# Performance work log

Measured on AMD Instinct MI355X. Metric: run time of the kernel, lower is better.

Reference implementation:

```python
import jax, jax.numpy as jnp
import numpy as np

G, P, PO, TAU = 4, 32, 128, 2.0  # n_groups, spatial_points, out_points=P*out_multiplier, level-softmax temperature
STRIDES = (4.0, 8.0, 16.0, 32.0)
EPS = 1e-5

def _ln2(x):
    # LayerNorm over last two dims, no affine (F.layer_norm(x, x.shape[-2:]))
    mu = jnp.mean(x, axis=(-2, -1), keepdims=True)
    var = jnp.var(x, axis=(-2, -1), keepdims=True)
    return (x - mu) * jax.lax.rsqrt(var + EPS)

def _ln1(x, g, b):
    mu = jnp.mean(x, axis=-1, keepdims=True)
    var = jnp.var(x, axis=-1, keepdims=True)
    return (x - mu) * jax.lax.rsqrt(var + EPS) * g + b

def _bilinear(feat, xp, yp):
    # feat: (B,G,H,W,Ce); xp,yp: (B,N,G,P) pixel coords; grid_sample bilinear,
    # zero padding, align_corners=False semantics.
    B, Gg, H, W, Ce = feat.shape
    x0 = jnp.floor(xp); y0 = jnp.floor(yp)
    wx1 = xp - x0; wy1 = yp - y0
    b_idx = jnp.arange(B)[:, None, None, None]
    g_idx = jnp.arange(Gg)[None, None, :, None]
    def gather(xi, yi):
        valid = (xi >= 0) & (xi < W) & (yi >= 0) & (yi < H)
        xc = jnp.clip(xi, 0, W - 1).astype(jnp.int32)
        yc = jnp.clip(yi, 0, H - 1).astype(jnp.int32)
        return feat[b_idx, g_idx, yc, xc] * valid[..., None]
    v00 = gather(x0, y0); v10 = gather(x0 + 1.0, y0)
    v01 = gather(x0, y0 + 1.0); v11 = gather(x0 + 1.0, y0 + 1.0)
    wx0 = 1.0 - wx1; wy0 = 1.0 - wy1
    return (v00 * (wx0 * wy0)[..., None] + v10 * (wx1 * wy0)[..., None]
            + v01 * (wx0 * wy1)[..., None] + v11 * (wx1 * wy1)[..., None])

def _forward(queries, xyzr, feats, W_off, b_off, W_param, b_param, W_out, b_out, gamma, beta):
    B, N, D = queries.shape
    Ce = feats[0].shape[1] // G  # 64 channels per group
    # learned offsets -> sample points (make_sample_points)
    offset = (queries @ W_off + b_off).reshape(B, N, G, P, 3)
    xy = xyzr[..., :2]
    z = xyzr[..., 2]
    r = xyzr[..., 3:4]
    roi_wh = (2.0 ** xyzr[..., 2:3]) * (2.0 ** jnp.concatenate([-0.5 * r, 0.5 * r], axis=-1))  # (B,N,2)
    sample_xy = xy[:, :, None, None, :] + offset[..., :2] * roi_wh[:, :, None, None, :]  # (B,N,G,P,2)
    sample_z = z[:, :, None, None] + offset[..., 2]  # (B,N,G,P) log2 scale
    # soft level assignment across the FPN pyramid
    lvl_log = jnp.log2(jnp.asarray(STRIDES, dtype=queries.dtype))
    lw = jax.nn.softmax(-((sample_z[..., None] - lvl_log) ** 2) / TAU, axis=-1)  # (B,N,G,P,L)
    # SAMPLE4D (image mode, T=1): multi-scale group-wise bilinear gather, level-weighted sum
    sampled = jnp.zeros((B, N, G, P, Ce), queries.dtype)
    for l, feat in enumerate(feats):
        H, W = feat.shape[-2:]
        featg = feat.reshape(B, G, Ce, H, W).transpose(0, 1, 3, 4, 2)  # (B,G,H,W,Ce)
        xp = sample_xy[..., 0] / STRIDES[l] - 0.5
        yp = sample_xy[..., 1] / STRIDES[l] - 0.5
        sampled = sampled + _bilinear(featg, xp, yp) * lw[..., l, None]
    # AdaptiveMixing: per-query generated channel-mix M and point-mix S
    params = (queries @ W_param + b_param).reshape(B, N, G, -1)
    M = params[..., :Ce * Ce].reshape(B, N, G, Ce, Ce)
    S = params[..., Ce * Ce:].reshape(B, N, G, PO, P)
    h = jnp.einsum('bngpc,bngcd->bngpd', sampled, M)  # channel mixing
    h = jax.nn.relu(_ln2(h))
    h = jnp.einsum('bngqp,bngpd->bngqd', S, h)        # point mixing -> (B,N,G,PO,Ce)
    h = jax.nn.relu(_ln2(h))
    h = h.reshape(B, N, G * PO * Ce)
    q = queries + h @ W_out + b_out  # out_proj + residual
    return _ln1(q, gamma, beta)      # norm_s

def setup_inputs() -> dict:
    key = jax.random.key(0)
    ks = jax.random.split(key, 12)
    B, N, D, C = 2, 300, 256, 256
    HW = [(200, 336), (100, 168), (50, 84), (25, 42)]
    inp = {}
    inp['queries'] = jax.random.normal(ks[0], (B, N, D), jnp.float32)
    u = jax.random.uniform(ks[1], (B, N, 4), jnp.float32)
    inp['xyzr'] = jnp.stack([u[..., 0] * 1344.0, u[..., 1] * 800.0,
                             2.0 + 3.0 * u[..., 2], u[..., 3] - 0.5], axis=-1)
    for i, (H, W) in enumerate(HW):
        inp[f'feat{i}'] = jax.random.normal(ks[2 + i], (B, C, H, W), jnp.float32)
    npar = G * (64 * 64 + PO * P)  # 32768
    inp['W_off'] = jax.random.normal(ks[6], (D, G * P * 3), jnp.float32) * 0.02
    inp['b_off'] = jax.random.normal(ks[7], (G * P * 3,), jnp.float32) * 0.1
    inp['W_param'] = jax.random.normal(ks[8], (D, npar), jnp.float32) * (1.0 / np.sqrt(D))
    inp['b_param'] = jnp.zeros((npar,), jnp.float32)
    inp['W_out'] = jax.random.normal(ks[9], (G * PO * 64, D), jnp.float32) * (1.0 / np.sqrt(G * PO * 64))
    inp['b_out'] = jnp.zeros((D,), jnp.float32)
    inp['gamma'] = jnp.ones((D,), jnp.float32)
    inp['beta'] = jnp.zeros((D,), jnp.float32)
    return inp

def reference(queries, xyzr, feat0, feat1, feat2, feat3, W_off, b_off, W_param, b_param, W_out, b_out, gamma, beta):
    return _forward(queries, xyzr, (feat0, feat1, feat2, feat3),
                    W_off, b_off, W_param, b_param, W_out, b_out, gamma, beta)
```

## Files before the change

### kernel.cpp

```cpp
#include <hip/hip_runtime.h>
#include <hip/hip_bf16.h>

typedef short bf16x8 __attribute__((ext_vector_type(8)));
typedef float f32x4 __attribute__((ext_vector_type(4)));
typedef unsigned short u16x4 __attribute__((ext_vector_type(4)));

#define NQ 600
#define D 256
#define NPAR 32768
#define EPS 1e-5f
#define KSPLIT 32

#define OFF_OFFS     ((size_t)0)
#define OFF_QB       ((size_t)1048576)
#define OFF_WOFFT    ((size_t)1441792)
#define OFF_H        ((size_t)2097152)
#define OFF_WPT      ((size_t)2097152)
#define OFF_PARAMS   ((size_t)41418752)
#define OFF_KPART    ((size_t)41418752)
#define OFF_WOT      ((size_t)80740352)
#define OFF_FEATT    ((size_t)97517568)

#define PIX_PER_BG 89250

__device__ __forceinline__ void gload_lds16(const void* g, void* l) {
    __builtin_amdgcn_global_load_lds((const __attribute__((address_space(1))) unsigned int*)g,
                                     (__attribute__((address_space(3))) unsigned int*)l,
                                     16, 0, 0);
}
__device__ __forceinline__ float bf2f(unsigned short us) {
    union { unsigned u; float f; } cv; cv.u = ((unsigned)us) << 16; return cv.f;
}
__device__ __forceinline__ unsigned short f2bf(float f) {
    __hip_bfloat16 h = __float2bfloat16(f);
    return *(unsigned short*)&h;
}

__global__ __launch_bounds__(256) void k_feat(
        const float* __restrict__ f0, const float* __restrict__ f1,
        const float* __restrict__ f2, const float* __restrict__ f3,
        __hip_bfloat16* __restrict__ featT) {
    int bid = blockIdx.x;
    int bg = bid / 349, wblk = bid % 349;
    int t = threadIdx.x, lane = t & 63, w = t >> 6;
    int wid = wblk * 4 + w;
    const float* in; int HW, lvloff, wstart;
    if (wid < 1050)      { in = f0; HW = 67200; lvloff = 0;     wstart = 0; }
    else if (wid < 1313) { in = f1; HW = 16800; lvloff = 67200; wstart = 1050; }
    else if (wid < 1379) { in = f2; HW = 4200;  lvloff = 84000; wstart = 1313; }
    else                 { in = f3; HW = 1050;  lvloff = 88200; wstart = 1379; }
    int b = bg >> 2, g = bg & 3;
    int pix = (wid - wstart) * 64 + lane;
    bool ok = pix < HW;
    int pixc = ok ? pix : HW - 1;
    const float* base = in + (size_t)(b * 256 + g * 64) * HW + pixc;
    float v[64];
    #pragma unroll
    for (int c = 0; c < 64; c++) v[c] = base[(size_t)c * HW];
    if (ok) {
        __hip_bfloat16* ob = featT + ((size_t)bg * PIX_PER_BG + lvloff + pixc) * 64;
        #pragma unroll
        for (int s8 = 0; s8 < 8; s8++) {
            unsigned short o[8];
            #pragma unroll
            for (int i = 0; i < 8; i++) o[i] = f2bf(v[s8 * 8 + i]);
            *(bf16x8*)(ob + s8 * 8) = *(bf16x8*)o;
        }
    }
}

__global__ __launch_bounds__(256) void k_wprep(
        const float* __restrict__ W_param, const float* __restrict__ W_out,
        const float* __restrict__ W_off, const float* __restrict__ q,
        __hip_bfloat16* __restrict__ Wpt, __hip_bfloat16* __restrict__ Wot,
        __hip_bfloat16* __restrict__ Wofft, __hip_bfloat16* __restrict__ qb) {
    __shared__ float tile[32][33];
    int idx = blockIdx.x;
    int t = threadIdx.x;
    if (idx >= 16480) {
        int i = (idx - 16480) * 2048 + t * 8;
        float4 v0 = *(const float4*)(q + i);
        float4 v1 = *(const float4*)(q + i + 4);
        unsigned short o[8];
        o[0] = f2bf(v0.x); o[1] = f2bf(v0.y); o[2] = f2bf(v0.z); o[3] = f2bf(v0.w);
        o[4] = f2bf(v1.x); o[5] = f2bf(v1.y); o[6] = f2bf(v1.z); o[7] = f2bf(v1.w);
        *(bf16x8*)(qb + i) = *(bf16x8*)o;
        return;
    }
    const float* in; __hip_bfloat16* out; int R, C, bx, by;
    if (idx < 8192)       { in = W_param; out = Wpt;   R = 256;   C = 32768; bx = idx & 1023; by = idx >> 10; }
    else if (idx < 16384) { idx -= 8192;  in = W_out;  out = Wot; R = 32768; C = 256; bx = idx & 7; by = idx >> 3; }
    else                  { idx -= 16384; in = W_off;  out = Wofft; R = 256; C = 384; bx = idx % 12; by = idx / 12; }
    int tx = t & 31, ty = t >> 5;
    int c = bx * 32 + tx;
    #pragma unroll
    for (int i = 0; i < 4; i++) {
        int rr = by * 32 + ty + i * 8;
        float v = 0.f;
        if (rr < R && c < C) v = in[(size_t)rr * C + c];
        tile[ty + i * 8][tx] = v;
    }
    __syncthreads();
    int r2 = by * 32 + tx;
    #pragma unroll
    for (int i = 0; i < 4; i++) {
        int c2 = bx * 32 + ty + i * 8;
        if (c2 < C && r2 < R) out[(size_t)c2 * R + r2] = __float2bfloat16(tile[tx][ty + i * 8]);
    }
}

__global__ __launch_bounds__(256) void k_gemm1_offs(const __hip_bfloat16* __restrict__ A,
                              const __hip_bfloat16* __restrict__ WofftB, const __hip_bfloat16* __restrict__ WptB,
                              const float* __restrict__ b_off, const float* __restrict__ b_param,
                              float* __restrict__ offs, __hip_bfloat16* __restrict__ params) {
    __shared__ __align__(16) char ldsB[32768];
    int id = blockIdx.x;
    bool isOff = id < 30;
    int m0, n0;
    const __hip_bfloat16* Bt;
    const float* bias;
    if (isOff) { m0 = (id % 5) * 128; n0 = (id / 5) * 64; Bt = WofftB; bias = b_off; }
    else { int i2 = id - 30; m0 = (i2 % 5) * 128; n0 = (i2 / 5) * 64; Bt = WptB; bias = b_param; }
    int t = threadIdx.x;
    int lane = t & 63, w = t >> 6;
    int la = lane & 15, lb = lane >> 4;

    const char* Bg = (const char*)Bt;
    #pragma unroll
    for (int r = 0; r < 8; r++) {
        int p = (r * 4 + w) * 64 + lane;
        int row = p >> 5, c16 = p & 31;
        int c16s = c16 ^ (row & 7);
        gload_lds16(Bg + (size_t)(n0 + row) * 512 + c16s * 16, ldsB + p * 16);
    }
    bf16x8 a[2][8];
    #pragma unroll
    for (int mi = 0; mi < 2; mi++) {
        int row = m0 + w * 32 + mi * 16 + la;
        row = row < NQ ? row : NQ - 1;
        #pragma unroll
        for (int ks = 0; ks < 8; ks++)
            a[mi][ks] = *(const bf16x8*)(A + (size_t)row * 256 + ks * 32 + lb * 8);
    }
    f32x4 acc[2][4];
    #pragma unroll
    for (int i = 0; i < 2; i++)
        #pragma unroll
        for (int j = 0; j < 4; j++) acc[i][j] = (f32x4)(0.f);
    __syncthreads();

    #pragma unroll
    for (int ks = 0; ks < 8; ks++) {
        bf16x8 b[4];
        #pragma unroll
        for (int ni = 0; ni < 4; ni++) {
            int row = ni * 16 + la;
            int c16s = (ks * 4 + lb) ^ (row & 7);
            b[ni] = *(const bf16x8*)(ldsB + row * 512 + c16s * 16);
        }
        #pragma unroll
        for (int mi = 0; mi < 2; mi++)
            #pragma unroll
            for (int ni = 0; ni < 4; ni++)
                acc[mi][ni] = __builtin_amdgcn_mfma_f32_16x16x32_bf16(a[mi][ks], b[ni], acc[mi][ni], 0, 0, 0);
    }
    #pragma unroll
    for (int mi = 0; mi < 2; mi++) {
        int rbase = m0 + w * 32 + mi * 16 + lb * 4;
        #pragma unroll
        for (int ni = 0; ni < 4; ni++) {
            int col = n0 + ni * 16 + la;
            float bv = bias[col];
            #pragma unroll
            for (int rg = 0; rg < 4; rg++) {
                int row = rbase + rg;
                if (row < NQ) {
                    if (isOff) offs[(size_t)row * 384 + col] = acc[mi][ni][rg] + bv;
                    else params[(size_t)row * NPAR + col] = __float2bfloat16(acc[mi][ni][rg] + bv);
                }
            }
        }
    }
}

#define MIX_SMP 0
#define MIX_MT  4096
#define MIX_SS  12288
#define MIX_H1T 20480
__device__ inline float2 blk_reduce2(float s, float ss, float* red, float norm) {
    __syncthreads();
    #pragma unroll
    for (int off = 32; off; off >>= 1) { s += __shfl_down(s, off); ss += __shfl_down(ss, off); }
    int wave = threadIdx.x >> 6, lane = threadIdx.x & 63;
    if (lane == 0) { red[wave * 2] = s; red[wave * 2 + 1] = ss; }
    __syncthreads();
    if (threadIdx.x == 0) {
        float a = 0.f, b = 0.f;
        #pragma unroll
        for (int i = 0; i < 4; i++) { a += red[2 * i]; b += red[2 * i + 1]; }
        red[8] = a * norm; red[9] = b * norm;
    }
    __syncthreads();
    return make_float2(red[8], red[9]);
}

__global__ __launch_bounds__(256) void k_sample_mix(const float* __restrict__ offs,
                      const float* __restrict__ xyzr,
                      const __hip_bfloat16* __restrict__ featT,
                      const __hip_bfloat16* __restrict__ params,
                      __hip_bfloat16* __restrict__ h) {
    __shared__ __align__(16) char lds[24576];
    __shared__ float smeta[32][8];
    __shared__ float red[16];
    int bid = blockIdx.x;
    int m = bid >> 2, g = bid & 3;
    int b = m / 300;
    int t = threadIdx.x;
    int lane = t & 63, w = t >> 6;
    int la = lane & 15, lb = lane >> 4;
    const __hip_bfloat16* pbase = params + (size_t)m * NPAR + g * 8192;

    #pragma unroll
    for (int r = 0; r < 2; r++) {
        int i = t + r * 256;
        int c = i >> 3, d0 = (i & 7) * 8;
        bf16x8 v = *(const bf16x8*)(pbase + i * 8);
        #pragma unroll
        for (int j = 0; j < 8; j++) {
            int d = d0 + j;
            int addr = MIX_MT + d * 128 + ((c >> 3) ^ (d & 7)) * 16 + (c & 7) * 2;
            *(unsigned short*)(lds + addr) = ((unsigned short*)&v)[j];
        }
    }
    #pragma unroll
    for (int r = 0; r < 2; r++) {
        int i = t + r * 256;
        int qr = i >> 2, c16 = i & 3;
        bf16x8 v = *(const bf16x8*)(pbase + 4096 + i * 8);
        *(bf16x8*)(lds + MIX_SS + qr * 64 + (c16 ^ (qr & 3)) * 16) = v;
    }
    if (t < 32) {
        int p = t;
        const float* op = offs + (size_t)m * 384 + (g * 32 + p) * 3;
        float o0 = op[0], o1 = op[1], o2 = op[2];
        float cx = xyzr[m * 4 + 0], cy = xyzr[m * 4 + 1], z = xyzr[m * 4 + 2], rr = xyzr[m * 4 + 3];
        smeta[p][0] = cx + o0 * exp2f(z - 0.5f * rr);
        smeta[p][1] = cy + o1 * exp2f(z + 0.5f * rr);
        float sz = z + o2;
        float e[4], mx = -1e30f;
        #pragma unroll
        for (int l = 0; l < 4; l++) { float d = sz - (float)(2 + l); e[l] = -0.5f * d * d; mx = fmaxf(mx, e[l]); }
        float ssum = 0.f;
        #pragma unroll
        for (int l = 0; l < 4; l++) { e[l] = __expf(e[l] - mx); ssum += e[l]; }
        float inv = 1.f / ssum;
        #pragma unroll
        for (int l = 0; l < 4; l++) smeta[p][2 + l] = e[l] * inv;
    }
    __syncthreads();

    int corner = lane >> 4;
    int dx = corner & 1, dy = corner >> 1;
    int ch = (lane & 15) * 4;
    const int Hs[4] = {200, 100, 50, 25};
    const int Ws[4] = {336, 168, 84, 42};
    const int Ls[4] = {0, 67200, 84000, 88200};
    const float invS[4] = {0.25f, 0.125f, 0.0625f, 0.03125f};
    const __hip_bfloat16* base_bg = featT + (size_t)(b * 4 + g) * PIX_PER_BG * 64;
    for (int pi = 0; pi < 8; pi++) {
        int p = w * 8 + pi;
        float sx = smeta[p][0], sy = smeta[p][1];
        float acc0 = 0.f, acc1 = 0.f, acc2 = 0.f, acc3 = 0.f;
        #pragma unroll
        for (int l = 0; l < 4; l++) {
            float wl = smeta[p][2 + l];
            if (wl < 1e-6f) continue;
            const int H = Hs[l], W = Ws[l];
            float xp = sx * invS[l] - 0.5f, yp = sy * invS[l] - 0.5f;
            float x0f = floorf(xp), y0f = floorf(yp);
            float wx1 = xp - x0f, wy1 = yp - y0f;
            int xi = (int)x0f + dx, yi = (int)y0f + dy;
            bool valid = (xi >= 0) && (xi < W) && (yi >= 0) && (yi < H);
            int xc = xi < 0 ? 0 : (xi >= W ? W - 1 : xi);
            int yc = yi < 0 ? 0 : (yi >= H ? H - 1 : yi);
            float cw = (dx ? wx1 : 1.f - wx1) * (dy ? wy1 : 1.f - wy1) * wl;
            if (!valid) cw = 0.f;
            const __hip_bfloat16* src = base_bg + ((size_t)Ls[l] + (size_t)yc * W + xc) * 64 + ch;
            u16x4 v = *(const u16x4*)src;
            acc0 += cw * bf2f(v[0]);
            acc1 += cw * bf2f(v[1]);
            acc2 += cw * bf2f(v[2]);
            acc3 += cw * bf2f(v[3]);
        }
        acc0 += __shfl_xor(acc0, 16); acc1 += __shfl_xor(acc1, 16);
        acc2 += __shfl_xor(acc2, 16); acc3 += __shfl_xor(acc3, 16);
        acc0 += __shfl_xor(acc0, 32); acc1 += __shfl_xor(acc1, 32);
        acc2 += __shfl_xor(acc2, 32); acc3 += __shfl_xor(acc3, 32);
        if (lane < 16) {
            unsigned short o[4];
            o[0] = f2bf(acc0); o[1] = f2bf(acc1); o[2] = f2bf(acc2); o[3] = f2bf(acc3);
            int slot = lane >> 1, half = lane & 1;
            *(u16x4*)(lds + MIX_SMP + p * 128 + ((slot ^ (p & 7)) * 16) + half * 8) = *(u16x4*)o;
        }
    }
    __syncthreads();

    f32x4 acc1v[2];
    acc1v[0] = (f32x4)(0.f); acc1v[1] = (f32x4)(0.f);
    int dcol = w * 16 + la;
    #pragma unroll
    for (int ks = 0; ks < 2; ks++) {
        bf16x8 bfr = *(const bf16x8*)(lds + MIX_MT + dcol * 128 + (((ks * 4 + lb)) ^ (dcol & 7)) * 16);
        #pragma unroll
        for (int mi = 0; mi < 2; mi++) {
            int prow = mi * 16 + la;
            bf16x8 afr = *(const bf16x8*)(lds + MIX_SMP + prow * 128 + ((ks * 4 + lb) ^ (prow & 7)) * 16);
            acc1v[mi] = __builtin_amdgcn_mfma_f32_16x16x32_bf16(afr, bfr, acc1v[mi], 0, 0, 0);
        }
    }
    float s = 0.f, ss = 0.f;
    #pragma unroll
    for (int mi = 0; mi < 2; mi++)
        #pragma unroll
        for (int j = 0; j < 4; j++) { float v = acc1v[mi][j]; s += v; ss += v * v; }
    float2 r1 = blk_reduce2(s, ss, red, 1.f / 2048.f);
    float mu = r1.x, inv = rsqrtf(r1.y - r1.x * r1.x + EPS);
    #pragma unroll
    for (int mi = 0; mi < 2; mi++) {
        u16x4 pk;
        #pragma unroll
        for (int rg = 0; rg < 4; rg++) {
            float v = (acc1v[mi][rg] - mu) * inv;
            pk[rg] = f2bf(v > 0.f ? v : 0.f);
        }
        int c16 = mi * 2 + (lb >> 1);
        int off8 = 8 * (lb & 1);
        *(u16x4*)(lds + MIX_H1T + dcol * 64 + ((c16 ^ (dcol & 3)) * 16) + off8) = pk;
    }
    __syncthreads();

    f32x4 acc2v[8];
    bf16x8 bfr2 = *(const bf16x8*)(lds + MIX_H1T + dcol * 64 + ((lb ^ (dcol & 3)) * 16));
    #pragma unroll
    for (int nj = 0; nj < 8; nj++) {
        int qrow = nj * 16 + la;
        bf16x8 afr = *(const bf16x8*)(lds + MIX_SS + qrow * 64 + ((lb ^ (qrow & 3)) * 16));
        acc2v[nj] = __builtin_amdgcn_mfma_f32_16x16x32_bf16(afr, bfr2, (f32x4)(0.f), 0, 0, 0);
    }
    s = 0.f; ss = 0.f;
    #pragma unroll
    for (int nj = 0; nj < 8; nj++)
        #pragma unroll
        for (int j = 0; j < 4; j++) { float v = acc2v[nj][j]; s += v; ss += v * v; }
    float2 r2 = blk_reduce2(s, ss, red, 1.f / 8192.f);
    float mu2 = r2.x, inv2 = rsqrtf(r2.y - r2.x * r2.x + EPS);
    __hip_bfloat16* hb = h + (size_t)m * NPAR + g * 8192;
    #pragma unroll
    for (int nj = 0; nj < 8; nj++) {
        #pragma unroll
        for (int rg = 0; rg < 4; rg++) {
            int qr = nj * 16 + lb * 4 + rg;
            float v = (acc2v[nj][rg] - mu2) * inv2;
            v = v > 0.f ? v : 0.f;
            hb[qr * 64 + dcol] = __float2bfloat16(v);
        }
    }
}

__global__ __launch_bounds__(256) void k_gemm_out(const __hip_bfloat16* __restrict__ A,
                           const __hip_bfloat16* __restrict__ Bt, float* __restrict__ kpart) {
    __shared__ __align__(16) char lds[49152];
    int bid = blockIdx.x;
    int work = (bid & 7) * 80 + (bid >> 3);
    int mblk = work % 10;
    int nz = work / 10;
    int n0 = (nz & 1) * 128;
    int z = nz >> 1;
    int m0 = mblk * 64;
    size_t k0 = (size_t)z * 1024;
    int t = threadIdx.x, lane = t & 63, w = t >> 6;
    int la = lane & 15, lb = lane >> 4;
    int wm = w >> 1, wn = w & 1;

    const char* Ag = (const char*)A;
    const char* Bg = (const char*)Bt;

    auto stage = [&](int buf, int st) {
        size_t kk = k0 + (size_t)st * 64;
        char* dstA = lds + buf * 24576;
        char* dstB = dstA + 8192;
        #pragma unroll
        for (int r = 0; r < 2; r++) {
            int p = (r * 4 + w) * 64 + lane;
            int row = p >> 3, c16 = p & 7;
            int c16s = c16 ^ (row & 7);
            int grow = m0 + row; grow = grow < NQ ? grow : NQ - 1;
            gload_lds16(Ag + ((size_t)grow * NPAR + kk) * 2 + c16s * 16, dstA + p * 16);
        }
        #pragma unroll
        for (int r = 0; r < 4; r++) {
            int p = (r * 4 + w) * 64 + lane;
            int row = p >> 3, c16 = p & 7;
            int c16s = c16 ^ (row & 7);
            gload_lds16(Bg + ((size_t)(n0 + row) * NPAR + kk) * 2 + c16s * 16, dstB + p * 16);
        }
    };

    f32x4 acc[2][4];
    #pragma unroll
    for (int i = 0; i < 2; i++)
        #pragma unroll
        for (int j = 0; j < 4; j++) acc[i][j] = (f32x4)(0.f);

    stage(0, 0);
    __syncthreads();
    for (int st = 0; st < 16; st++) {
        int buf = st & 1;
        if (st < 15) stage(buf ^ 1, st + 1);
        const char* tA = lds + buf * 24576;
        const char* tB = tA + 8192;
        #pragma unroll
        for (int ks = 0; ks < 2; ks++) {
            bf16x8 a[2], b[4];
            #pragma unroll
            for (int mi = 0; mi < 2; mi++) {
                int row = wm * 32 + mi * 16 + la;
                int c16s = (ks * 4 + lb) ^ (row & 7);
                a[mi] = *(const bf16x8*)(tA + row * 128 + c16s * 16);
            }
            #pragma unroll
            for (int ni = 0; ni < 4; ni++) {
                int row = wn * 64 + ni * 16 + la;
                int c16s = (ks * 4 + lb) ^ (row & 7);
                b[ni] = *(const bf16x8*)(tB + row * 128 + c16s * 16);
            }
            #pragma unroll
            for (int mi = 0; mi < 2; mi++)
                #pragma unroll
                for (int ni = 0; ni < 4; ni++)
                    acc[mi][ni] = __builtin_amdgcn_mfma_f32_16x16x32_bf16(a[mi], b[ni], acc[mi][ni], 0, 0, 0);
        }
        __syncthreads();
    }

    float* outp = kpart + (size_t)z * (NQ * D);
    #pragma unroll
    for (int mi = 0; mi < 2; mi++) {
        int rbase = m0 + wm * 32 + mi * 16 + lb * 4;
        #pragma unroll
        for (int ni = 0; ni < 4; ni++) {
            int col = n0 + wn * 64 + ni * 16 + la;
            #pragma unroll
            for (int rg = 0; rg < 4; rg++) {
                int row = rbase + rg;
                if (row < NQ) outp[(size_t)row * D + col] = acc[mi][ni][rg];
            }
        }
    }
}

__global__ void k_ln_out(const float* __restrict__ kpart, const float* __restrict__ queries,
                         const float* __restrict__ b_out, const float* __restrict__ gamma,
                         const float* __restrict__ beta, float* __restrict__ out) {
    int m = blockIdx.x, t = threadIdx.x;
    float x = queries[m * 256 + t] + b_out[t];
    for (int kc = 0; kc < KSPLIT; kc++) x += kpart[(size_t)kc * (NQ * D) + m * 256 + t];
    __shared__ float red[16];
    float s = x, ss = x * x;
    #pragma unroll
    for (int off = 32; off; off >>= 1) { s += __shfl_down(s, off); ss += __shfl_down(ss, off); }
    int wave = t >> 6, lane = t & 63;
    if (lane == 0) { red[wave * 2] = s; red[wave * 2 + 1] = ss; }
    __syncthreads();
    if (t == 0) {
        float a = 0.f, b = 0.f;
        #pragma unroll
        for (int i = 0; i < 4; i++) { a += red[2 * i]; b += red[2 * i + 1]; }
        red[8] = a * (1.f / 256.f); red[9] = b * (1.f / 256.f);
    }
    __syncthreads();
    float mu = red[8], var = red[9] - mu * mu;
    float inv = rsqrtf(var + EPS);
    out[m * 256 + t] = (x - mu) * inv * gamma[t] + beta[t];
}

extern "C" void kernel_launch(void* const* d_in, const int* in_sizes, int n_in,
                              void* d_out, int out_size, void* d_ws, size_t ws_size,
                              hipStream_t stream) {
    const float* queries = (const float*)d_in[0];
    const float* xyzr    = (const float*)d_in[1];
    const float* f0      = (const float*)d_in[2];
    const float* f1      = (const float*)d_in[3];
    const float* f2      = (const float*)d_in[4];
    const float* f3      = (const float*)d_in[5];
    const float* W_off   = (const float*)d_in[6];
    const float* b_off   = (const float*)d_in[7];
    const float* W_param = (const float*)d_in[8];
    const float* b_param = (const float*)d_in[9];
    const float* W_out   = (const float*)d_in[10];
    const float* b_out   = (const float*)d_in[11];
    const float* gamma   = (const float*)d_in[12];
    const float* beta    = (const float*)d_in[13];
    float* out = (float*)d_out;
    char* ws = (char*)d_ws;

    float* offs            = (float*)(ws + OFF_OFFS);
    __hip_bfloat16* qb     = (__hip_bfloat16*)(ws + OFF_QB);
    __hip_bfloat16* Wofft  = (__hip_bfloat16*)(ws + OFF_WOFFT);
    __hip_bfloat16* hbuf   = (__hip_bfloat16*)(ws + OFF_H);
    __hip_bfloat16* Wpt    = (__hip_bfloat16*)(ws + OFF_WPT);
    __hip_bfloat16* params = (__hip_bfloat16*)(ws + OFF_PARAMS);
    float* kpart           = (float*)(ws + OFF_KPART);
    __hip_bfloat16* Wot    = (__hip_bfloat16*)(ws + OFF_WOT);
    __hip_bfloat16* featT  = (__hip_bfloat16*)(ws + OFF_FEATT);

    k_feat<<<2792, 256, 0, stream>>>(f0, f1, f2, f3, featT);
    k_wprep<<<16555, 256, 0, stream>>>(W_param, W_out, W_off, queries, Wpt, Wot, Wofft, qb);
    k_gemm1_offs<<<2590, 256, 0, stream>>>(qb, Wofft, Wpt, b_off, b_param, offs, params);
    k_sample_mix<<<2400, 256, 0, stream>>>(offs, xyzr, featT, params, hbuf);
    k_gemm_out<<<640, 256, 0, stream>>>(hbuf, Wot, kpart);
    k_ln_out<<<600, 256, 0, stream>>>(kpart, queries, b_out, gamma, beta, out);
}
```

Before: 205.0 us.

## Fuse weight transpose into GEMM1 and merge feature and weight prep kernels

```diff
diff --git a/kernel.cpp b/kernel.cpp
--- a/kernel.cpp
+++ b/kernel.cpp
@@ -13,9 +13,7 @@
 
 #define OFF_OFFS     ((size_t)0)
 #define OFF_QB       ((size_t)1048576)
-#define OFF_WOFFT    ((size_t)1441792)
 #define OFF_H        ((size_t)2097152)
-#define OFF_WPT      ((size_t)2097152)
 #define OFF_PARAMS   ((size_t)41418752)
 #define OFF_KPART    ((size_t)41418752)
 #define OFF_WOT      ((size_t)80740352)
@@ -36,147 +34,148 @@
     return *(unsigned short*)&h;
 }
 
-__global__ __launch_bounds__(256) void k_feat(
+__global__ __launch_bounds__(256) void k_prep(
         const float* __restrict__ f0, const float* __restrict__ f1,
         const float* __restrict__ f2, const float* __restrict__ f3,
-        __hip_bfloat16* __restrict__ featT) {
+        const float* __restrict__ W_out, const float* __restrict__ q,
+        __hip_bfloat16* __restrict__ featT,
+        __hip_bfloat16* __restrict__ Wot, __hip_bfloat16* __restrict__ qb) {
+    __shared__ float tile[32][33];
     int bid = blockIdx.x;
-    int bg = bid / 349, wblk = bid % 349;
-    int t = threadIdx.x, lane = t & 63, w = t >> 6;
-    int wid = wblk * 4 + w;
-    const float* in; int HW, lvloff, wstart;
-    if (wid < 1050)      { in = f0; HW = 67200; lvloff = 0;     wstart = 0; }
-    else if (wid < 1313) { in = f1; HW = 16800; lvloff = 67200; wstart = 1050; }
-    else if (wid < 1379) { in = f2; HW = 4200;  lvloff = 84000; wstart = 1313; }
-    else                 { in = f3; HW = 1050;  lvloff = 88200; wstart = 1379; }
-    int b = bg >> 2, g = bg & 3;
-    int pix = (wid - wstart) * 64 + lane;
-    bool ok = pix < HW;
-    int pixc = ok ? pix : HW - 1;
-    const float* base = in + (size_t)(b * 256 + g * 64) * HW + pixc;
-    float v[64];
-    #pragma unroll
-    for (int c = 0; c < 64; c++) v[c] = base[(size_t)c * HW];
-    if (ok) {
-        __hip_bfloat16* ob = featT + ((size_t)bg * PIX_PER_BG + lvloff + pixc) * 64;
-        #pragma unroll
-        for (int s8 = 0; s8 < 8; s8++) {
-            unsigned short o[8];
-            #pragma unroll
-            for (int i = 0; i < 8; i++) o[i] = f2bf(v[s8 * 8 + i]);
-            *(bf16x8*)(ob + s8 * 8) = *(bf16x8*)o;
-        }
-    }
-}
-
-__global__ __launch_bounds__(256) void k_wprep(
-        const float* __restrict__ W_param, const float* __restrict__ W_out,
-        const float* __restrict__ W_off, const float* __restrict__ q,
-        __hip_bfloat16* __restrict__ Wpt, __hip_bfloat16* __restrict__ Wot,
-        __hip_bfloat16* __restrict__ Wofft, __hip_bfloat16* __restrict__ qb) {
-    __shared__ float tile[32][33];
-    int idx = blockIdx.x;
     int t = threadIdx.x;
-    if (idx >= 16480) {
-        int i = (idx - 16480) * 2048 + t * 8;
-        float4 v0 = *(const float4*)(q + i);
-        float4 v1 = *(const float4*)(q + i + 4);
-        unsigned short o[8];
-        o[0] = f2bf(v0.x); o[1] = f2bf(v0.y); o[2] = f2bf(v0.z); o[3] = f2bf(v0.w);
-        o[4] = f2bf(v1.x); o[5] = f2bf(v1.y); o[6] = f2bf(v1.z); o[7] = f2bf(v1.w);
-        *(bf16x8*)(qb + i) = *(bf16x8*)o;
+    if (bid < 2792) {
+        int bg = bid / 349, wblk = bid % 349;
+        int lane = t & 63, w = t >> 6;
+        int wid = wblk * 4 + w;
+        const float* in; int HW, lvloff, wstart;
+        if (wid < 1050)      { in = f0; HW = 67200; lvloff = 0;     wstart = 0; }
+        else if (wid < 1313) { in = f1; HW = 16800; lvloff = 67200; wstart = 1050; }
+        else if (wid < 1379) { in = f2; HW = 4200;  lvloff = 84000; wstart = 1313; }
+        else                 { in = f3; HW = 1050;  lvloff = 88200; wstart = 1379; }
+        int b = bg >> 2, g = bg & 3;
+        int pix = (wid - wstart) * 64 + lane;
+        bool ok = pix < HW;
+        int pixc = ok ? pix : HW - 1;
+        const float* base = in + (size_t)(b * 256 + g * 64) * HW + pixc;
+        float v[64];
+        #pragma unroll
+        for (int c = 0; c < 64; c++) v[c] = base[(size_t)c * HW];
+        if (ok) {
+            __hip_bfloat16* ob = featT + ((size_t)bg * PIX_PER_BG + lvloff + pixc) * 64;
+            #pragma unroll
+            for (int s8 = 0; s8 < 8; s8++) {
+                unsigned short o[8];
+                #pragma unroll
+                for (int i = 0; i < 8; i++) o[i] = f2bf(v[s8 * 8 + i]);
+                *(bf16x8*)(ob + s8 * 8) = *(bf16x8*)o;
+            }
+        }
         return;
     }
-    const float* in; __hip_bfloat16* out; int R, C, bx, by;
-    if (idx < 8192)       { in = W_param; out = Wpt;   R = 256;   C = 32768; bx = idx & 1023; by = idx >> 10; }
-    else if (idx < 16384) { idx -= 8192;  in = W_out;  out = Wot; R = 32768; C = 256; bx = idx & 7; by = idx >> 3; }
-    else                  { idx -= 16384; in = W_off;  out = Wofft; R = 256; C = 384; bx = idx % 12; by = idx / 12; }
-    int tx = t & 31, ty = t >> 5;
-    int c = bx * 32 + tx;
-    #pragma unroll
-    for (int i = 0; i < 4; i++) {
-        int rr = by * 32 + ty + i * 8;
-        float v = 0.f;
-        if (rr < R && c < C) v = in[(size_t)rr * C + c];
-        tile[ty + i * 8][tx] = v;
-    }
-    __syncthreads();
-    int r2 = by * 32 + tx;
-    #pragma unroll
-    for (int i = 0; i < 4; i++) {
-        int c2 = bx * 32 + ty + i * 8;
-        if (c2 < C && r2 < R) out[(size_t)c2 * R + r2] = __float2bfloat16(tile[tx][ty + i * 8]);
-    }
-}
-
-__global__ __launch_bounds__(256) void k_gemm1_offs(const __hip_bfloat16* __restrict__ A,
-                              const __hip_bfloat16* __restrict__ WofftB, const __hip_bfloat16* __restrict__ WptB,
+    int idx = bid - 2792;
+    if (idx < 8192) {
+        int bx = idx & 7, by = idx >> 3;
+        const int R = 32768, C = 256;
+        int tx = t & 31, ty = t >> 5;
+        int c = bx * 32 + tx;
+        #pragma unroll
+        for (int i = 0; i < 4; i++) {
+            int rr = by * 32 + ty + i * 8;
+            tile[ty + i * 8][tx] = W_out[(size_t)rr * C + c];
+        }
+        __syncthreads();
+        int r2 = by * 32 + tx;
+        #pragma unroll
+        for (int i = 0; i < 4; i++) {
+            int c2 = bx * 32 + ty + i * 8;
+            Wot[(size_t)c2 * R + r2] = __float2bfloat16(tile[tx][ty + i * 8]);
+        }
+        return;
+    }
+    int i = (idx - 8192) * 2048 + t * 8;
+    float4 v0 = *(const float4*)(q + i);
+    float4 v1 = *(const float4*)(q + i + 4);
+    unsigned short o[8];
+    o[0] = f2bf(v0.x); o[1] = f2bf(v0.y); o[2] = f2bf(v0.z); o[3] = f2bf(v0.w);
+    o[4] = f2bf(v1.x); o[5] = f2bf(v1.y); o[6] = f2bf(v1.z); o[7] = f2bf(v1.w);
+    *(bf16x8*)(qb + i) = *(bf16x8*)o;
+}
+
+__global__ __launch_bounds__(256) void k_gemm1(const __hip_bfloat16* __restrict__ A,
+                              const float* __restrict__ W_off, const float* __restrict__ W_param,
                               const float* __restrict__ b_off, const float* __restrict__ b_param,
                               float* __restrict__ offs, __hip_bfloat16* __restrict__ params) {
     __shared__ __align__(16) char ldsB[32768];
     int id = blockIdx.x;
-    bool isOff = id < 30;
-    int m0, n0;
-    const __hip_bfloat16* Bt;
-    const float* bias;
-    if (isOff) { m0 = (id % 5) * 128; n0 = (id / 5) * 64; Bt = WofftB; bias = b_off; }
-    else { int i2 = id - 30; m0 = (i2 % 5) * 128; n0 = (i2 / 5) * 64; Bt = WptB; bias = b_param; }
+    bool isOff = id < 6;
+    const float* Wsrc; const float* bias; int n0; size_t C;
+    if (isOff) { Wsrc = W_off; bias = b_off; n0 = id * 64; C = 384; }
+    else { Wsrc = W_param; bias = b_param; n0 = (id - 6) * 64; C = 32768; }
     int t = threadIdx.x;
     int lane = t & 63, w = t >> 6;
     int la = lane & 15, lb = lane >> 4;
 
-    const char* Bg = (const char*)Bt;
-    #pragma unroll
-    for (int r = 0; r < 8; r++) {
-        int p = (r * 4 + w) * 64 + lane;
-        int row = p >> 5, c16 = p & 31;
-        int c16s = c16 ^ (row & 7);
-        gload_lds16(Bg + (size_t)(n0 + row) * 512 + c16s * 16, ldsB + p * 16);
-    }
-    bf16x8 a[2][8];
-    #pragma unroll
-    for (int mi = 0; mi < 2; mi++) {
-        int row = m0 + w * 32 + mi * 16 + la;
-        row = row < NQ ? row : NQ - 1;
-        #pragma unroll
-        for (int ks = 0; ks < 8; ks++)
-            a[mi][ks] = *(const bf16x8*)(A + (size_t)row * 256 + ks * 32 + lb * 8);
-    }
-    f32x4 acc[2][4];
-    #pragma unroll
-    for (int i = 0; i < 2; i++)
-        #pragma unroll
-        for (int j = 0; j < 4; j++) acc[i][j] = (f32x4)(0.f);
-    __syncthreads();
-
-    #pragma unroll
-    for (int ks = 0; ks < 8; ks++) {
-        bf16x8 b[4];
-        #pragma unroll
-        for (int ni = 0; ni < 4; ni++) {
-            int row = ni * 16 + la;
-            int c16s = (ks * 4 + lb) ^ (row & 7);
-            b[ni] = *(const bf16x8*)(ldsB + row * 512 + c16s * 16);
-        }
-        #pragma unroll
-        for (int mi = 0; mi < 2; mi++)
-            #pragma unroll
-            for (int ni = 0; ni < 4; ni++)
-                acc[mi][ni] = __builtin_amdgcn_mfma_f32_16x16x32_bf16(a[mi][ks], b[ni], acc[mi][ni], 0, 0, 0);
-    }
-    #pragma unroll
-    for (int mi = 0; mi < 2; mi++) {
-        int rbase = m0 + w * 32 + mi * 16 + lb * 4;
-        #pragma unroll
-        for (int ni = 0; ni < 4; ni++) {
-            int col = n0 + ni * 16 + la;
-            float bv = bias[col];
-            #pragma unroll
-            for (int rg = 0; rg < 4; rg++) {
-                int row = rbase + rg;
-                if (row < NQ) {
-                    if (isOff) offs[(size_t)row * 384 + col] = acc[mi][ni][rg] + bv;
-                    else params[(size_t)row * NPAR + col] = __float2bfloat16(acc[mi][ni][rg] + bv);
+    #pragma unroll
+    for (int i = 0; i < 16; i++) {
+        int kk = i * 16 + w * 4 + (lane >> 4);
+        int j4 = (lane & 15) * 4;
+        float4 v = *(const float4*)(Wsrc + (size_t)kk * C + n0 + j4);
+        float vv[4] = {v.x, v.y, v.z, v.w};
+        #pragma unroll
+        for (int u = 0; u < 4; u++) {
+            int j = j4 + u;
+            int addr = j * 512 + (((kk >> 3) ^ (j & 7)) * 16) + (kk & 7) * 2;
+            *(unsigned short*)(ldsB + addr) = f2bf(vv[u]);
+        }
+    }
+    __syncthreads();
+
+    #pragma unroll 1
+    for (int mt = 0; mt < 5; mt++) {
+        int m0 = mt * 128;
+        bf16x8 a[2][8];
+        #pragma unroll
+        for (int mi = 0; mi < 2; mi++) {
+            int row = m0 + w * 32 + mi * 16 + la;
+            row = row < NQ ? row : NQ - 1;
+            #pragma unroll
+            for (int ks = 0; ks < 8; ks++)
+                a[mi][ks] = *(const bf16x8*)(A + (size_t)row * 256 + ks * 32 + lb * 8);
+        }
+        f32x4 acc[2][4];
+        #pragma unroll
+        for (int i = 0; i < 2; i++)
+            #pragma unroll
+            for (int j = 0; j < 4; j++) acc[i][j] = (f32x4)(0.f);
+        #pragma unroll
+        for (int ks = 0; ks < 8; ks++) {
+            bf16x8 b[4];
+            #pragma unroll
+            for (int ni = 0; ni < 4; ni++) {
+                int row = ni * 16 + la;
+                int c16s = (ks * 4 + lb) ^ (row & 7);
+                b[ni] = *(const bf16x8*)(ldsB + row * 512 + c16s * 16);
+            }
+            #pragma unroll
+            for (int mi = 0; mi < 2; mi++)
+                #pragma unroll
+                for (int ni = 0; ni < 4; ni++)
+                    acc[mi][ni] = __builtin_amdgcn_mfma_f32_16x16x32_bf16(a[mi][ks], b[ni], acc[mi][ni], 0, 0, 0);
+        }
+        #pragma unroll
+        for (int mi = 0; mi < 2; mi++) {
+            int rbase = m0 + w * 32 + mi * 16 + lb * 4;
+            #pragma unroll
+            for (int ni = 0; ni < 4; ni++) {
+                int col = n0 + ni * 16 + la;
+                float bv = bias[col];
+                #pragma unroll
+                for (int rg = 0; rg < 4; rg++) {
+                    int row = rbase + rg;
+                    if (row < NQ) {
+                        if (isOff) offs[(size_t)row * 384 + col] = acc[mi][ni][rg] + bv;
+                        else params[(size_t)row * NPAR + col] = __float2bfloat16(acc[mi][ni][rg] + bv);
+                    }
                 }
             }
         }
@@ -506,17 +505,14 @@
 
     float* offs            = (float*)(ws + OFF_OFFS);
     __hip_bfloat16* qb     = (__hip_bfloat16*)(ws + OFF_QB);
-    __hip_bfloat16* Wofft  = (__hip_bfloat16*)(ws + OFF_WOFFT);
     __hip_bfloat16* hbuf   = (__hip_bfloat16*)(ws + OFF_H);
-    __hip_bfloat16* Wpt    = (__hip_bfloat16*)(ws + OFF_WPT);
     __hip_bfloat16* params = (__hip_bfloat16*)(ws + OFF_PARAMS);
     float* kpart           = (float*)(ws + OFF_KPART);
     __hip_bfloat16* Wot    = (__hip_bfloat16*)(ws + OFF_WOT);
     __hip_bfloat16* featT  = (__hip_bfloat16*)(ws + OFF_FEATT);
 
-    k_feat<<<2792, 256, 0, stream>>>(f0, f1, f2, f3, featT);
-    k_wprep<<<16555, 256, 0, stream>>>(W_param, W_out, W_off, queries, Wpt, Wot, Wofft, qb);
-    k_gemm1_offs<<<2590, 256, 0, stream>>>(qb, Wofft, Wpt, b_off, b_param, offs, params);
+    k_prep<<<11059, 256, 0, stream>>>(f0, f1, f2, f3, W_out, queries, featT, Wot, qb);
+    k_gemm1<<<518, 256, 0, stream>>>(qb, W_off, W_param, b_off, b_param, offs, params);
     k_sample_mix<<<2400, 256, 0, stream>>>(offs, xyzr, featT, params, hbuf);
     k_gemm_out<<<640, 256, 0, stream>>>(hbuf, Wot, kpart);
     k_ln_out<<<600, 256, 0, stream>>>(kpart, queries, b_out, gamma, beta, out);
```

Measured after the change: 189.5 us (median of 2 runs). 7.6% less time.
